# Performance work log

Hardware: AMD Instinct MI355X
Metric: run time of the kernel (lower is better)

The kernel has to match this reference:

```python
import jax, jax.numpy as jnp
import numpy as np

N, E, D, H = 100000, 1600000, 128, 2  # nodes, edges, channels (in=out), heads
NEG_SLOPE = 0.2
EPS = 1e-16


def setup_inputs() -> dict:
    key = jax.random.key(0)
    ks = jax.random.split(key, 12)
    s = 1.0 / np.sqrt(D)
    return {
        "x": jax.random.normal(ks[0], (N, D), jnp.float32),
        "edge_index": jax.random.randint(ks[1], (2, E), 0, N, jnp.int64),
        "gamma": jnp.ones((D,), jnp.float32),
        "beta": jnp.zeros((D,), jnp.float32),
        "Wl": jax.random.normal(ks[2], (D, H * D), jnp.float32) * s,
        "bl": jnp.zeros((H * D,), jnp.float32),
        "Wr": jax.random.normal(ks[3], (D, H * D), jnp.float32) * s,
        "br": jnp.zeros((H * D,), jnp.float32),
        "att": jax.random.normal(ks[4], (H, D), jnp.float32) * s,
        "res_W": jax.random.normal(ks[5], (D, D), jnp.float32) * s,
        "bias": jnp.zeros((D,), jnp.float32),
    }


def _segment_softmax(alpha, seg, num_segments):
    m = jax.ops.segment_max(alpha, seg, num_segments=num_segments)
    a = jnp.exp(alpha - m[seg])
    z = jax.ops.segment_sum(a, seg, num_segments=num_segments)
    return a / (z[seg] + EPS)


def reference(x, edge_index, gamma, beta, Wl, bl, Wr, br, att, res_W, bias):
    n = x.shape[0]
    residual = x
    # per-node LayerNorm -> ReLU
    mu = x.mean(-1, keepdims=True)
    var = ((x - mu) ** 2).mean(-1, keepdims=True)
    h = (x - mu) * jax.lax.rsqrt(var + 1e-5) * gamma + beta
    h = jax.nn.relu(h)
    # GATv2: per-node linear transforms [N,H,D]
    xl = (h @ Wl + bl).reshape(n, H, D)  # source-side
    xr = (h @ Wr + br).reshape(n, H, D)  # target-side
    src, dst = edge_index[0], edge_index[1]
    e = jax.nn.leaky_relu(xl[src] + xr[dst], NEG_SLOPE)  # [E,H,D]
    alpha = jnp.einsum('ehd,hd->eh', e, att)             # [E,H]
    alpha = _segment_softmax(alpha, dst, n)
    msg = xl[src] * alpha[..., None]                     # [E,H,D]
    out = jax.ops.segment_sum(msg, dst, num_segments=n)  # [N,H,D]
    out = out.mean(axis=1)                               # concat=False -> mean heads
    out = out + h @ res_W + bias                         # GATv2 internal residual + bias
    return residual + out
```

## Files before the change

kernel.cpp:

```cpp
#include <hip/hip_runtime.h>
#include <hip/hip_bf16.h>
#include <cstdint>
#include <cstddef>

#define DCH 128
#define NHEADS 2
#define NEG_SLOPE 0.2f

typedef __attribute__((ext_vector_type(8))) short short8v;
typedef __attribute__((ext_vector_type(4))) float f32x4;
typedef __attribute__((ext_vector_type(2))) float f32x2;
typedef __attribute__((ext_vector_type(4))) int int4v;
typedef _Float16 h4 __attribute__((ext_vector_type(4)));

__device__ __forceinline__ unsigned short f2bf(float f) {
    union { float f; unsigned int i; } v; v.f = f;
    unsigned int r = v.i + 0x7fffu + ((v.i >> 16) & 1u);
    return (unsigned short)(r >> 16);
}
__device__ __forceinline__ unsigned short f2h_bits(float f) {
    _Float16 h = (_Float16)f;
    union { _Float16 h; unsigned short u; } v; v.h = h; return v.u;
}

__device__ __forceinline__ float halfsum(float p) {
    p += __int_as_float(__builtin_amdgcn_update_dpp(
            0, __float_as_int(p), 0x121, 0xF, 0xF, false));
    p += __int_as_float(__builtin_amdgcn_update_dpp(
            0, __float_as_int(p), 0x122, 0xF, 0xF, false));
    p += __int_as_float(__builtin_amdgcn_update_dpp(
            0, __float_as_int(p), 0x124, 0xF, 0xF, false));
    p += __int_as_float(__builtin_amdgcn_update_dpp(
            0, __float_as_int(p), 0x128, 0xF, 0xF, false));
    p += __int_as_float(__builtin_amdgcn_ds_swizzle(
            __float_as_int(p), 0x401F));
    return p;
}

__global__ void prep_hist(const float* __restrict__ Wl, const float* __restrict__ Wr,
                          const float* __restrict__ resW,
                          unsigned short* __restrict__ wfrag,
                          const int* __restrict__ dst, int* __restrict__ cnt, int E) {
    if (blockIdx.x >= 40) {
        int i = (blockIdx.x - 40) * 256 + threadIdx.x;
        int E4 = E >> 2;
        if (i < E4) {
            int4 d = ((const int4*)dst)[i];
            atomicAdd(&cnt[d.x], 1); atomicAdd(&cnt[d.y], 1);
            atomicAdd(&cnt[d.z], 1); atomicAdd(&cnt[d.w], 1);
        }
        if (i < (E & 3)) atomicAdd(&cnt[dst[E4 * 4 + i]], 1);
        return;
    }
    int gid  = blockIdx.x * 256 + threadIdx.x;
    int lane = gid & 63;
    int f    = gid >> 6;
    int ks   = f & 3;
    int ct   = f >> 2;
    int col  = ct * 16 + (lane & 15);
    int k0   = ks * 32 + (lane >> 4) * 8;
    const float* W; int ldB, c;
    if (col < 256)      { W = Wl;   ldB = 256; c = col; }
    else if (col < 512) { W = Wr;   ldB = 256; c = col - 256; }
    else                { W = resW; ldB = 128; c = col - 512; }
    unsigned short tmp[8];
#pragma unroll
    for (int j = 0; j < 8; ++j) tmp[j] = f2bf(W[(size_t)(k0 + j) * ldB + c]);
    ushort4* dstp = (ushort4*)(wfrag + (size_t)gid * 8);
    dstp[0] = make_ushort4(tmp[0], tmp[1], tmp[2], tmp[3]);
    dstp[1] = make_ushort4(tmp[4], tmp[5], tmp[6], tmp[7]);
}

__launch_bounds__(256)
__global__ void gemm_fill(const float* __restrict__ x,
                          const float* __restrict__ gamma, const float* __restrict__ beta,
                          const unsigned short* __restrict__ wfrag,
                          const float* __restrict__ bl, const float* __restrict__ br,
                          const float* __restrict__ bias,
                          unsigned char* __restrict__ xl8, unsigned short* __restrict__ xr,
                          float* __restrict__ out, int n,
                          const int* __restrict__ srcIdx, const int* __restrict__ dstIdx,
                          int* __restrict__ fillc, int* __restrict__ sbuf, int E, int nrb) {
    __shared__ __align__(16) unsigned char smem[128 * 256];

    if ((int)blockIdx.x >= nrb) {
        int i = (blockIdx.x - nrb) * 256 + threadIdx.x;
        int E4 = E >> 2;
        if (i < E4) {
            int4 d = ((const int4*)dstIdx)[i];
            int4 s = ((const int4*)srcIdx)[i];
            sbuf[atomicAdd(&fillc[d.x], 1)] = s.x;
            sbuf[atomicAdd(&fillc[d.y], 1)] = s.y;
            sbuf[atomicAdd(&fillc[d.z], 1)] = s.z;
            sbuf[atomicAdd(&fillc[d.w], 1)] = s.w;
        }
        if (i < (E & 3)) {
            int e = E4 * 4 + i;
            sbuf[atomicAdd(&fillc[dstIdx[e]], 1)] = srcIdx[e];
        }
        return;
    }

    int row0 = blockIdx.x * 128;
    int tid  = threadIdx.x;
    unsigned short* As = (unsigned short*)smem;

    {
        int r  = tid >> 5;
        int k4 = (tid & 31) * 4;
        float4 g4  = *(const float4*)(gamma + k4);
        float4 be4 = *(const float4*)(beta + k4);
#pragma unroll
        for (int i = 0; i < 16; ++i) {
            int row  = r + i * 8;
            int grow = row0 + row;
            float4 a = (grow < n) ? *(const float4*)(x + (size_t)grow * DCH + k4)
                                  : make_float4(0.f, 0.f, 0.f, 0.f);
            float s  = a.x + a.y + a.z + a.w;
            float sq = a.x * a.x + a.y * a.y + a.z * a.z + a.w * a.w;
#pragma unroll
            for (int msk = 16; msk; msk >>= 1) {
                s  += __shfl_xor(s, msk);
                sq += __shfl_xor(sq, msk);
            }
            float mu = s * (1.f / DCH);
            float rs = rsqrtf(sq * (1.f / DCH) - mu * mu + 1e-5f);
            ushort4 u;
            u.x = f2bf(fmaxf((a.x - mu) * rs * g4.x + be4.x, 0.f));
            u.y = f2bf(fmaxf((a.y - mu) * rs * g4.y + be4.y, 0.f));
            u.z = f2bf(fmaxf((a.z - mu) * rs * g4.z + be4.z, 0.f));
            u.w = f2bf(fmaxf((a.w - mu) * rs * g4.w + be4.w, 0.f));
            int byteoff = row * 256 + ((k4 * 2) ^ ((row & 7) << 4));
            *(ushort4*)((char*)As + byteoff) = u;
        }
    }
    __syncthreads();

    int wv = tid >> 6, lane = tid & 63;

    short8v afrag[2][4];
#pragma unroll
    for (int g = 0; g < 2; ++g) {
        int arow = wv * 32 + g * 16 + (lane & 15);
#pragma unroll
        for (int ks = 0; ks < 4; ++ks) {
            int kbyte = (ks * 64 + (lane >> 4) * 16) ^ ((arow & 7) << 4);
            afrag[g][ks] = *(const short8v*)((const char*)As + arow * 256 + kbyte);
        }
    }
    __syncthreads();

    int nodeL0 = wv * 32 + (lane & 15);
    int nodeL1 = nodeL0 + 16;
    int cq = (lane >> 4) << 2;

    auto mfma_ct = [&](int ct, f32x4& a0, f32x4& a1) {
        const unsigned short* bp = wfrag + ((size_t)(ct * 4) * 64 + lane) * 8;
        short8v b0 = *(const short8v*)(bp);
        short8v b1 = *(const short8v*)(bp + 64 * 8);
        short8v b2 = *(const short8v*)(bp + 128 * 8);
        short8v b3 = *(const short8v*)(bp + 192 * 8);
        a0 = __builtin_amdgcn_mfma_f32_16x16x32_bf16(b0, afrag[0][0], a0, 0, 0, 0);
        a1 = __builtin_amdgcn_mfma_f32_16x16x32_bf16(b0, afrag[1][0], a1, 0, 0, 0);
        a0 = __builtin_amdgcn_mfma_f32_16x16x32_bf16(b1, afrag[0][1], a0, 0, 0, 0);
        a1 = __builtin_amdgcn_mfma_f32_16x16x32_bf16(b1, afrag[1][1], a1, 0, 0, 0);
        a0 = __builtin_amdgcn_mfma_f32_16x16x32_bf16(b2, afrag[0][2], a0, 0, 0, 0);
        a1 = __builtin_amdgcn_mfma_f32_16x16x32_bf16(b2, afrag[1][2], a1, 0, 0, 0);
        a0 = __builtin_amdgcn_mfma_f32_16x16x32_bf16(b3, afrag[0][3], a0, 0, 0, 0);
        a1 = __builtin_amdgcn_mfma_f32_16x16x32_bf16(b3, afrag[1][3], a1, 0, 0, 0);
    };

    {
#pragma unroll
        for (int ct = 0; ct < 16; ++ct) {
            f32x4 a0 = {0,0,0,0}, a1 = {0,0,0,0};
            mfma_ct(ct, a0, a1);
            int c = ct * 16 + cq;
            float4 bb = *(const float4*)(bl + c);
            int cb = ct * 16 + cq;
            int p0 = __builtin_amdgcn_cvt_pk_fp8_f32(a0[0] + bb.x, a0[1] + bb.y, 0, false);
            p0     = __builtin_amdgcn_cvt_pk_fp8_f32(a0[2] + bb.z, a0[3] + bb.w, p0, true);
            *(int*)(smem + nodeL0 * 256 + (cb ^ ((nodeL0 & 7) << 4))) = p0;
            int p1 = __builtin_amdgcn_cvt_pk_fp8_f32(a1[0] + bb.x, a1[1] + bb.y, 0, false);
            p1     = __builtin_amdgcn_cvt_pk_fp8_f32(a1[2] + bb.z, a1[3] + bb.w, p1, true);
            *(int*)(smem + nodeL1 * 256 + (cb ^ ((nodeL1 & 7) << 4))) = p1;
        }
        __syncthreads();
#pragma unroll
        for (int it = 0; it < 8; ++it) {
            int chunk = it * 256 + tid;
            int row  = chunk >> 4;
            int colb = (chunk & 15) * 16;
            int grow = row0 + row;
            if (grow < n) {
                int4v v = *(const int4v*)(smem + row * 256 + (colb ^ ((row & 7) << 4)));
                *(int4v*)(xl8 + (size_t)grow * 256 + colb) = v;
            }
        }
        __syncthreads();
    }

    for (int fg = 0; fg < 2; ++fg) {
#pragma unroll
        for (int ctl = 0; ctl < 8; ++ctl) {
            int ct = 16 + fg * 8 + ctl;
            f32x4 a0 = {0,0,0,0}, a1 = {0,0,0,0};
            mfma_ct(ct, a0, a1);
            int c = ct * 16 + cq - 256;
            float4 bb = *(const float4*)(br + c);
            int cb = ctl * 32 + cq * 2;
            ushort4 u0 = make_ushort4(f2h_bits(a0[0] + bb.x), f2h_bits(a0[1] + bb.y),
                                      f2h_bits(a0[2] + bb.z), f2h_bits(a0[3] + bb.w));
            *(ushort4*)(smem + nodeL0 * 256 + (cb ^ ((nodeL0 & 7) << 4))) = u0;
            ushort4 u1 = make_ushort4(f2h_bits(a1[0] + bb.x), f2h_bits(a1[1] + bb.y),
                                      f2h_bits(a1[2] + bb.z), f2h_bits(a1[3] + bb.w));
            *(ushort4*)(smem + nodeL1 * 256 + (cb ^ ((nodeL1 & 7) << 4))) = u1;
        }
        __syncthreads();
#pragma unroll
        for (int it = 0; it < 8; ++it) {
            int chunk = it * 256 + tid;
            int row  = chunk >> 4;
            int colb = (chunk & 15) * 16;
            int grow = row0 + row;
            if (grow < n) {
                int4v v = *(const int4v*)(smem + row * 256 + (colb ^ ((row & 7) << 4)));
                __builtin_nontemporal_store(v,
                    (int4v*)((char*)xr + (size_t)grow * 512 + fg * 256 + colb));
            }
        }
        __syncthreads();
    }

    for (int fg = 0; fg < 2; ++fg) {
#pragma unroll
        for (int ctl = 0; ctl < 4; ++ctl) {
            int ct = 32 + fg * 4 + ctl;
            f32x4 a0 = {0,0,0,0}, a1 = {0,0,0,0};
            mfma_ct(ct, a0, a1);
            int c = ct * 16 + cq - 512;
            float4 bb = *(const float4*)(bias + c);
            int cb = ctl * 64 + cq * 4;
            float4 w0 = make_float4(a0[0] + bb.x, a0[1] + bb.y,
                                    a0[2] + bb.z, a0[3] + bb.w);
            *(float4*)(smem + nodeL0 * 256 + (cb ^ ((nodeL0 & 7) << 4))) = w0;
            float4 w1 = make_float4(a1[0] + bb.x, a1[1] + bb.y,
                                    a1[2] + bb.z, a1[3] + bb.w);
            *(float4*)(smem + nodeL1 * 256 + (cb ^ ((nodeL1 & 7) << 4))) = w1;
        }
        __syncthreads();
#pragma unroll
        for (int it = 0; it < 8; ++it) {
            int chunk = it * 256 + tid;
            int row  = chunk >> 4;
            int colb = (chunk & 15) * 16;
            int grow = row0 + row;
            if (grow < n) {
                f32x4 v = *(const f32x4*)(smem + row * 256 + (colb ^ ((row & 7) << 4)));
                const float* xp = (const float*)((const char*)x + (size_t)grow * 512 + fg * 256 + colb);
                f32x4 xv = *(const f32x4*)xp;
                v = v + xv;
                __builtin_nontemporal_store(v,
                    (f32x4*)((char*)out + (size_t)grow * 512 + fg * 256 + colb));
            }
        }
        __syncthreads();
    }
}

__global__ void scan_block(const int* __restrict__ cnt, int* __restrict__ offs,
                           int* __restrict__ bsum, int n) {
    __shared__ int sm[256];
    int t = threadIdx.x;
    int i = blockIdx.x * 256 + t;
    int v = (i < n) ? cnt[i] : 0;
    sm[t] = v;
    __syncthreads();
#pragma unroll
    for (int d = 1; d < 256; d <<= 1) {
        int add = (t >= d) ? sm[t - d] : 0;
        __syncthreads();
        sm[t] += add;
        __syncthreads();
    }
    if (i < n) offs[i] = sm[t] - v;
    if (t == 255) bsum[blockIdx.x] = sm[t];
}

__global__ void scan_bsum_par(int* __restrict__ bsum, int nb) {
    __shared__ int sm[512];
    int t = threadIdx.x;
    if (nb <= 512) {
        int v = (t < nb) ? bsum[t] : 0;
        sm[t] = v;
        __syncthreads();
#pragma unroll
        for (int d = 1; d < 512; d <<= 1) {
            int add = (t >= d) ? sm[t - d] : 0;
            __syncthreads();
            sm[t] += add;
            __syncthreads();
        }
        if (t < nb) bsum[t] = sm[t] - v;
    } else if (t == 0) {
        int acc = 0;
        for (int i = 0; i < nb; ++i) { int v = bsum[i]; bsum[i] = acc; acc += v; }
    }
}

__global__ void scan_add(int* __restrict__ offs, int* __restrict__ fillc,
                         const int* __restrict__ bsum, int n, int E) {
    int i = blockIdx.x * 256 + threadIdx.x;
    if (i < n) {
        int v = offs[i] + bsum[blockIdx.x];
        offs[i]  = v;
        fillc[i] = v;
    }
    if (i == 0) offs[n] = E;
}

__launch_bounds__(256)
__global__ void gat_aggregate(const int* __restrict__ offs, const int* __restrict__ sbuf,
                              const unsigned char* __restrict__ xl8,
                              const unsigned short* __restrict__ xr_,
                              const float* __restrict__ att,
                              float* __restrict__ out, int n) {
    const _Float16* xr = (const _Float16*)xr_;
    int lane = threadIdx.x & 63;
    int wid  = __builtin_amdgcn_readfirstlane((blockIdx.x * blockDim.x + threadIdx.x) >> 6);
    int nw   = (gridDim.x * blockDim.x) >> 6;

    const float LOG2E = 1.4426950408889634f;
    float4 af = *(const float4*)(att + lane * 4);
    float ax = af.x * LOG2E, ay = af.y * LOG2E, az = af.z * LOG2E, aw = af.w * LOG2E;

    for (int t = wid; t < n; t += nw) {
        int beg = offs[t];
        int end = offs[t + 1];
        if (beg == end) continue;
        h4 rr = *(const h4*)(xr + (size_t)t * 256 + lane * 4);
        float rx = (float)rr[0], ry = (float)rr[1], rz = (float)rr[2], rw = (float)rr[3];

        float m = -INFINITY, z = 0.f;
        float4 acc = make_float4(0.f, 0.f, 0.f, 0.f);

        auto process4 = [&](int u0, int u1, int u2, int u3) {
            f32x2 l0a = __builtin_amdgcn_cvt_pk_f32_fp8(u0, false);
            f32x2 l0b = __builtin_amdgcn_cvt_pk_f32_fp8(u0, true);
            f32x2 l1a = __builtin_amdgcn_cvt_pk_f32_fp8(u1, false);
            f32x2 l1b = __builtin_amdgcn_cvt_pk_f32_fp8(u1, true);
            f32x2 l2a = __builtin_amdgcn_cvt_pk_f32_fp8(u2, false);
            f32x2 l2b = __builtin_amdgcn_cvt_pk_f32_fp8(u2, true);
            f32x2 l3a = __builtin_amdgcn_cvt_pk_f32_fp8(u3, false);
            f32x2 l3b = __builtin_amdgcn_cvt_pk_f32_fp8(u3, true);

            auto logit = [&](f32x2 la, f32x2 lb) {
                float vx = la.x + rx; vx = fmaxf(vx, NEG_SLOPE * vx);
                float vy = la.y + ry; vy = fmaxf(vy, NEG_SLOPE * vy);
                float vz = lb.x + rz; vz = fmaxf(vz, NEG_SLOPE * vz);
                float vw = lb.y + rw; vw = fmaxf(vw, NEG_SLOPE * vw);
                return fmaf(vw, aw, fmaf(vz, az, fmaf(vy, ay, vx * ax)));
            };
            float p0 = halfsum(logit(l0a, l0b));
            float p1 = halfsum(logit(l1a, l1b));
            float p2 = halfsum(logit(l2a, l2b));
            float p3 = halfsum(logit(l3a, l3b));
            float pm = fmaxf(fmaxf(p0, p1), fmaxf(p2, p3));
            if (__any(pm - m > 11.5f)) {
                float mn = fmaxf(m, pm);
                float sc = __builtin_amdgcn_exp2f(m - mn);
                z *= sc;
                acc.x *= sc; acc.y *= sc; acc.z *= sc; acc.w *= sc;
                m = mn;
            }
            float w0 = __builtin_amdgcn_exp2f(p0 - m);
            float w1 = __builtin_amdgcn_exp2f(p1 - m);
            float w2 = __builtin_amdgcn_exp2f(p2 - m);
            float w3 = __builtin_amdgcn_exp2f(p3 - m);
            z += (w0 + w1) + (w2 + w3);
            acc.x = fmaf(l0a.x, w0, acc.x); acc.y = fmaf(l0a.y, w0, acc.y);
            acc.z = fmaf(l0b.x, w0, acc.z); acc.w = fmaf(l0b.y, w0, acc.w);
            acc.x = fmaf(l1a.x, w1, acc.x); acc.y = fmaf(l1a.y, w1, acc.y);
            acc.z = fmaf(l1b.x, w1, acc.z); acc.w = fmaf(l1b.y, w1, acc.w);
            acc.x = fmaf(l2a.x, w2, acc.x); acc.y = fmaf(l2a.y, w2, acc.y);
            acc.z = fmaf(l2b.x, w2, acc.z); acc.w = fmaf(l2b.y, w2, acc.w);
            acc.x = fmaf(l3a.x, w3, acc.x); acc.y = fmaf(l3a.y, w3, acc.y);
            acc.z = fmaf(l3b.x, w3, acc.z); acc.w = fmaf(l3b.y, w3, acc.w);
        };

        int j = beg;
        int c0, c1, c2, c3;
        int d0, d1, d2, d3;
        bool haveC = (j + 4 <= end);
        if (haveC) {
            int s0 = sbuf[j], s1 = sbuf[j + 1], s2 = sbuf[j + 2], s3 = sbuf[j + 3];
            c0 = *(const int*)(xl8 + (size_t)s0 * 256 + lane * 4);
            c1 = *(const int*)(xl8 + (size_t)s1 * 256 + lane * 4);
            c2 = *(const int*)(xl8 + (size_t)s2 * 256 + lane * 4);
            c3 = *(const int*)(xl8 + (size_t)s3 * 256 + lane * 4);
        }
        bool haveD = (j + 8 <= end);
        if (haveD) {
            int s0 = sbuf[j + 4], s1 = sbuf[j + 5], s2 = sbuf[j + 6], s3 = sbuf[j + 7];
            d0 = *(const int*)(xl8 + (size_t)s0 * 256 + lane * 4);
            d1 = *(const int*)(xl8 + (size_t)s1 * 256 + lane * 4);
            d2 = *(const int*)(xl8 + (size_t)s2 * 256 + lane * 4);
            d3 = *(const int*)(xl8 + (size_t)s3 * 256 + lane * 4);
        }
        for (; j + 12 <= end; j += 4) {
            int s0 = sbuf[j + 8], s1 = sbuf[j + 9], s2 = sbuf[j + 10], s3 = sbuf[j + 11];
            int n0 = *(const int*)(xl8 + (size_t)s0 * 256 + lane * 4);
            int n1 = *(const int*)(xl8 + (size_t)s1 * 256 + lane * 4);
            int n2 = *(const int*)(xl8 + (size_t)s2 * 256 + lane * 4);
            int n3 = *(const int*)(xl8 + (size_t)s3 * 256 + lane * 4);
            process4(c0, c1, c2, c3);
            c0 = d0; c1 = d1; c2 = d2; c3 = d3;
            d0 = n0; d1 = n1; d2 = n2; d3 = n3;
        }
        if (haveD) {
            process4(c0, c1, c2, c3);
            c0 = d0; c1 = d1; c2 = d2; c3 = d3;
            j += 4;
        }
        if (haveC) {
            process4(c0, c1, c2, c3);
            j += 4;
        }
        for (; j < end; ++j) {
            int u = *(const int*)(xl8 + (size_t)sbuf[j] * 256 + lane * 4);
            f32x2 la = __builtin_amdgcn_cvt_pk_f32_fp8(u, false);
            f32x2 lb = __builtin_amdgcn_cvt_pk_f32_fp8(u, true);
            float vx = la.x + rx; vx = fmaxf(vx, NEG_SLOPE * vx);
            float vy = la.y + ry; vy = fmaxf(vy, NEG_SLOPE * vy);
            float vz = lb.x + rz; vz = fmaxf(vz, NEG_SLOPE * vz);
            float vw = lb.y + rw; vw = fmaxf(vw, NEG_SLOPE * vw);
            float p = halfsum(fmaf(vw, aw, fmaf(vz, az, fmaf(vy, ay, vx * ax))));
            if (__any(p - m > 11.5f)) {
                float mn = fmaxf(m, p);
                float sc = __builtin_amdgcn_exp2f(m - mn);
                z *= sc;
                acc.x *= sc; acc.y *= sc; acc.z *= sc; acc.w *= sc;
                m = mn;
            }
            float w = __builtin_amdgcn_exp2f(p - m);
            z += w;
            acc.x = fmaf(la.x, w, acc.x); acc.y = fmaf(la.y, w, acc.y);
            acc.z = fmaf(lb.x, w, acc.z); acc.w = fmaf(lb.y, w, acc.w);
        }
        float inv = 0.5f / (z + 1e-16f);
        acc.x *= inv; acc.y *= inv; acc.z *= inv; acc.w *= inv;
        acc.x += __shfl_xor(acc.x, 32);
        acc.y += __shfl_xor(acc.y, 32);
        acc.z += __shfl_xor(acc.z, 32);
        acc.w += __shfl_xor(acc.w, 32);
        if (lane < 32) {
            float4* o = (float4*)(out + (size_t)t * DCH + lane * 4);
            float4 cur = *o;
            cur.x += acc.x; cur.y += acc.y; cur.z += acc.z; cur.w += acc.w;
            *o = cur;
        }
    }
}

extern "C" void kernel_launch(void* const* d_in, const int* in_sizes, int n_in,
                              void* d_out, int out_size, void* d_ws, size_t ws_size,
                              hipStream_t stream) {
    const float* x     = (const float*)d_in[0];
    const int*   ei    = (const int*)d_in[1];
    const float* gamma = (const float*)d_in[2];
    const float* beta  = (const float*)d_in[3];
    const float* Wl    = (const float*)d_in[4];
    const float* bl    = (const float*)d_in[5];
    const float* Wr    = (const float*)d_in[6];
    const float* br    = (const float*)d_in[7];
    const float* att   = (const float*)d_in[8];
    const float* resW  = (const float*)d_in[9];
    const float* bias  = (const float*)d_in[10];
    float* out = (float*)d_out;

    int n = in_sizes[0] / DCH;
    int E = in_sizes[1] / 2;
    const int* src = ei;
    const int* dstIdx = ei + E;

    char* ws = (char*)d_ws;
    size_t off = 0;
    auto alloc = [&](size_t bytes) -> void* {
        void* p = ws + off;
        off = (off + bytes + 255) & ~(size_t)255;
        return p;
    };

    int nb = (n + 255) / 256;

    unsigned char*  xl8 = (unsigned char*)alloc((size_t)n * 256);
    unsigned short* xr  = (unsigned short*)alloc((size_t)n * 256 * 2);
    unsigned short* wfrag = (unsigned short*)alloc(160 * 64 * 8 * 2);
    int* cnt   = (int*)alloc((size_t)n * 4);
    int* offs  = (int*)alloc((size_t)(n + 1) * 4);
    int* bsum  = (int*)alloc((size_t)nb * 4);
    int* fillc = (int*)alloc((size_t)n * 4);
    int* sbuf  = (int*)alloc((size_t)E * 4);

    (void)hipMemsetAsync(cnt, 0, (size_t)n * 4, stream);
    int ethr = (E / 4 + 255) / 256 + 1;
    prep_hist<<<40 + ethr, 256, 0, stream>>>(Wl, Wr, resW, wfrag, dstIdx, cnt, E);
    scan_block<<<nb, 256, 0, stream>>>(cnt, offs, bsum, n);
    scan_bsum_par<<<1, 512, 0, stream>>>(bsum, nb);
    scan_add<<<nb, 256, 0, stream>>>(offs, fillc, bsum, n, E);

    int nrb = (n + 127) / 128;
    gemm_fill<<<nrb + ethr, 256, 0, stream>>>(x, gamma, beta, wfrag, bl, br, bias,
                                              xl8, xr, out, n,
                                              src, dstIdx, fillc, sbuf, E, nrb);
    gat_aggregate<<<2048, 256, 0, stream>>>(offs, sbuf, xl8, xr, att, out, n);
}
```

Measured before the change: 290.7 us.

## Overlap edge histogram with GEMM and run CSR fill standalone

Moves the per-destination degree histogram out of the weight-prep kernel and into the GEMM kernel's extra blocks. The CSR fill becomes its own kernel that runs after the scan. This swaps which edge pass overlaps with the dense GEMM: the cheaper histogram now hides behind GEMM, while the heavier scatter fill runs alone. Weight prep becomes a small separate launch, which adds one kernel launch.

New measurement: 355.9 us. +22.4%, slower.

```diff
diff --git a/kernel.cpp b/kernel.cpp
--- a/kernel.cpp
+++ b/kernel.cpp
@@ -37,21 +37,9 @@
     return p;
 }
 
-__global__ void prep_hist(const float* __restrict__ Wl, const float* __restrict__ Wr,
-                          const float* __restrict__ resW,
-                          unsigned short* __restrict__ wfrag,
-                          const int* __restrict__ dst, int* __restrict__ cnt, int E) {
-    if (blockIdx.x >= 40) {
-        int i = (blockIdx.x - 40) * 256 + threadIdx.x;
-        int E4 = E >> 2;
-        if (i < E4) {
-            int4 d = ((const int4*)dst)[i];
-            atomicAdd(&cnt[d.x], 1); atomicAdd(&cnt[d.y], 1);
-            atomicAdd(&cnt[d.z], 1); atomicAdd(&cnt[d.w], 1);
-        }
-        if (i < (E & 3)) atomicAdd(&cnt[dst[E4 * 4 + i]], 1);
-        return;
-    }
+__global__ void prep_wfrag(const float* __restrict__ Wl, const float* __restrict__ Wr,
+                           const float* __restrict__ resW,
+                           unsigned short* __restrict__ wfrag) {
     int gid  = blockIdx.x * 256 + threadIdx.x;
     int lane = gid & 63;
     int f    = gid >> 6;
@@ -72,15 +60,15 @@
 }
 
 __launch_bounds__(256)
-__global__ void gemm_fill(const float* __restrict__ x,
+__global__ void gemm_hist(const float* __restrict__ x,
                           const float* __restrict__ gamma, const float* __restrict__ beta,
                           const unsigned short* __restrict__ wfrag,
                           const float* __restrict__ bl, const float* __restrict__ br,
                           const float* __restrict__ bias,
                           unsigned char* __restrict__ xl8, unsigned short* __restrict__ xr,
                           float* __restrict__ out, int n,
-                          const int* __restrict__ srcIdx, const int* __restrict__ dstIdx,
-                          int* __restrict__ fillc, int* __restrict__ sbuf, int E, int nrb) {
+                          const int* __restrict__ dstIdx, int* __restrict__ cnt,
+                          int E, int nrb) {
     __shared__ __align__(16) unsigned char smem[128 * 256];
 
     if ((int)blockIdx.x >= nrb) {
@@ -88,16 +76,10 @@
         int E4 = E >> 2;
         if (i < E4) {
             int4 d = ((const int4*)dstIdx)[i];
-            int4 s = ((const int4*)srcIdx)[i];
-            sbuf[atomicAdd(&fillc[d.x], 1)] = s.x;
-            sbuf[atomicAdd(&fillc[d.y], 1)] = s.y;
-            sbuf[atomicAdd(&fillc[d.z], 1)] = s.z;
-            sbuf[atomicAdd(&fillc[d.w], 1)] = s.w;
-        }
-        if (i < (E & 3)) {
-            int e = E4 * 4 + i;
-            sbuf[atomicAdd(&fillc[dstIdx[e]], 1)] = srcIdx[e];
-        }
+            atomicAdd(&cnt[d.x], 1); atomicAdd(&cnt[d.y], 1);
+            atomicAdd(&cnt[d.z], 1); atomicAdd(&cnt[d.w], 1);
+        }
+        if (i < (E & 3)) atomicAdd(&cnt[dstIdx[E4 * 4 + i]], 1);
         return;
     }
 
@@ -317,6 +299,24 @@
         fillc[i] = v;
     }
     if (i == 0) offs[n] = E;
+}
+
+__global__ void fill_csr(const int* __restrict__ src, const int* __restrict__ dst,
+                         int* __restrict__ fillc, int* __restrict__ sbuf, int E) {
+    int i = blockIdx.x * blockDim.x + threadIdx.x;
+    int E4 = E >> 2;
+    if (i < E4) {
+        int4 d = ((const int4*)dst)[i];
+        int4 s = ((const int4*)src)[i];
+        sbuf[atomicAdd(&fillc[d.x], 1)] = s.x;
+        sbuf[atomicAdd(&fillc[d.y], 1)] = s.y;
+        sbuf[atomicAdd(&fillc[d.z], 1)] = s.z;
+        sbuf[atomicAdd(&fillc[d.w], 1)] = s.w;
+    }
+    if (i < (E & 3)) {
+        int e = E4 * 4 + i;
+        sbuf[atomicAdd(&fillc[dst[e]], 1)] = src[e];
+    }
 }
 
 __launch_bounds__(256)
@@ -503,15 +503,15 @@
     int* sbuf  = (int*)alloc((size_t)E * 4);
 
     (void)hipMemsetAsync(cnt, 0, (size_t)n * 4, stream);
+    prep_wfrag<<<40, 256, 0, stream>>>(Wl, Wr, resW, wfrag);
+
+    int nrb = (n + 127) / 128;
     int ethr = (E / 4 + 255) / 256 + 1;
-    prep_hist<<<40 + ethr, 256, 0, stream>>>(Wl, Wr, resW, wfrag, dstIdx, cnt, E);
+    gemm_hist<<<nrb + ethr, 256, 0, stream>>>(x, gamma, beta, wfrag, bl, br, bias,
+                                              xl8, xr, out, n, dstIdx, cnt, E, nrb);
     scan_block<<<nb, 256, 0, stream>>>(cnt, offs, bsum, n);
     scan_bsum_par<<<1, 512, 0, stream>>>(bsum, nb);
     scan_add<<<nb, 256, 0, stream>>>(offs, fillc, bsum, n, E);
-
-    int nrb = (n + 127) / 128;
-    gemm_fill<<<nrb + ethr, 256, 0, stream>>>(x, gamma, beta, wfrag, bl, br, bias,
-                                              xl8, xr, out, n,
-                                              src, dstIdx, fillc, sbuf, E, nrb);
+    fill_csr<<<ethr, 256, 0, stream>>>(src, dstIdx, fillc, sbuf, E);
     gat_aggregate<<<2048, 256, 0, stream>>>(offs, sbuf, xl8, xr, att, out, n);
 }
```

## Split CSR fill by destination half and overlap second half with aggregation

Applied to the files above, without the earlier changes.

The CSR fill is split in two by destination node. The first half is filled alongside the GEMM. The second half is filled by extra blocks in a new fused kernel that at the same time aggregates the first-half nodes, and a final kernel then aggregates the second half. The aim is to hide the atomic scatter cost behind aggregation work. In exchange, the edge lists are read twice and there is one more kernel launch.

After: 308.1 us. 6.0% more time.

```diff
diff --git a/kernel.cpp b/kernel.cpp
--- a/kernel.cpp
+++ b/kernel.cpp
@@ -80,7 +80,8 @@
                           unsigned char* __restrict__ xl8, unsigned short* __restrict__ xr,
                           float* __restrict__ out, int n,
                           const int* __restrict__ srcIdx, const int* __restrict__ dstIdx,
-                          int* __restrict__ fillc, int* __restrict__ sbuf, int E, int nrb) {
+                          int* __restrict__ fillc, int* __restrict__ sbuf, int E,
+                          int nrb, int nhalf) {
     __shared__ __align__(16) unsigned char smem[128 * 256];
 
     if ((int)blockIdx.x >= nrb) {
@@ -89,14 +90,15 @@
         if (i < E4) {
             int4 d = ((const int4*)dstIdx)[i];
             int4 s = ((const int4*)srcIdx)[i];
-            sbuf[atomicAdd(&fillc[d.x], 1)] = s.x;
-            sbuf[atomicAdd(&fillc[d.y], 1)] = s.y;
-            sbuf[atomicAdd(&fillc[d.z], 1)] = s.z;
-            sbuf[atomicAdd(&fillc[d.w], 1)] = s.w;
+            if (d.x < nhalf) sbuf[atomicAdd(&fillc[d.x], 1)] = s.x;
+            if (d.y < nhalf) sbuf[atomicAdd(&fillc[d.y], 1)] = s.y;
+            if (d.z < nhalf) sbuf[atomicAdd(&fillc[d.z], 1)] = s.z;
+            if (d.w < nhalf) sbuf[atomicAdd(&fillc[d.w], 1)] = s.w;
         }
         if (i < (E & 3)) {
             int e = E4 * 4 + i;
-            sbuf[atomicAdd(&fillc[dstIdx[e]], 1)] = srcIdx[e];
+            int d = dstIdx[e];
+            if (d < nhalf) sbuf[atomicAdd(&fillc[d], 1)] = srcIdx[e];
         }
         return;
     }
@@ -319,22 +321,16 @@
     if (i == 0) offs[n] = E;
 }
 
-__launch_bounds__(256)
-__global__ void gat_aggregate(const int* __restrict__ offs, const int* __restrict__ sbuf,
-                              const unsigned char* __restrict__ xl8,
-                              const unsigned short* __restrict__ xr_,
-                              const float* __restrict__ att,
-                              float* __restrict__ out, int n) {
-    const _Float16* xr = (const _Float16*)xr_;
-    int lane = threadIdx.x & 63;
-    int wid  = __builtin_amdgcn_readfirstlane((blockIdx.x * blockDim.x + threadIdx.x) >> 6);
-    int nw   = (gridDim.x * blockDim.x) >> 6;
-
+__device__ __forceinline__ void gat_range(
+        const int* __restrict__ offs, const int* __restrict__ sbuf,
+        const unsigned char* __restrict__ xl8, const _Float16* __restrict__ xr,
+        const float* __restrict__ att, float* __restrict__ out,
+        int t0, int t1, int wid, int nw, int lane) {
     const float LOG2E = 1.4426950408889634f;
     float4 af = *(const float4*)(att + lane * 4);
     float ax = af.x * LOG2E, ay = af.y * LOG2E, az = af.z * LOG2E, aw = af.w * LOG2E;
 
-    for (int t = wid; t < n; t += nw) {
+    for (int t = t0 + wid; t < t1; t += nw) {
         int beg = offs[t];
         int end = offs[t + 1];
         if (beg == end) continue;
@@ -462,6 +458,50 @@
     }
 }
 
+__launch_bounds__(256)
+__global__ void gat_fill(const int* __restrict__ offs, const int* __restrict__ sbuf,
+                         const unsigned char* __restrict__ xl8,
+                         const unsigned short* __restrict__ xr_,
+                         const float* __restrict__ att, float* __restrict__ out,
+                         const int* __restrict__ srcIdx, const int* __restrict__ dstIdx,
+                         int* __restrict__ fillc, int* __restrict__ sbufW,
+                         int E, int nhalf, int GB) {
+    if ((int)blockIdx.x >= GB) {
+        int i = (blockIdx.x - GB) * 256 + threadIdx.x;
+        int E4 = E >> 2;
+        if (i < E4) {
+            int4 d = ((const int4*)dstIdx)[i];
+            int4 s = ((const int4*)srcIdx)[i];
+            if (d.x >= nhalf) sbufW[atomicAdd(&fillc[d.x], 1)] = s.x;
+            if (d.y >= nhalf) sbufW[atomicAdd(&fillc[d.y], 1)] = s.y;
+            if (d.z >= nhalf) sbufW[atomicAdd(&fillc[d.z], 1)] = s.z;
+            if (d.w >= nhalf) sbufW[atomicAdd(&fillc[d.w], 1)] = s.w;
+        }
+        if (i < (E & 3)) {
+            int e = E4 * 4 + i;
+            int d = dstIdx[e];
+            if (d >= nhalf) sbufW[atomicAdd(&fillc[d], 1)] = srcIdx[e];
+        }
+        return;
+    }
+    int lane = threadIdx.x & 63;
+    int wid  = __builtin_amdgcn_readfirstlane((blockIdx.x * 256 + threadIdx.x) >> 6);
+    int nw   = GB * 4;
+    gat_range(offs, sbuf, xl8, (const _Float16*)xr_, att, out, 0, nhalf, wid, nw, lane);
+}
+
+__launch_bounds__(256)
+__global__ void gat_aggregate(const int* __restrict__ offs, const int* __restrict__ sbuf,
+                              const unsigned char* __restrict__ xl8,
+                              const unsigned short* __restrict__ xr_,
+                              const float* __restrict__ att,
+                              float* __restrict__ out, int t0, int t1) {
+    int lane = threadIdx.x & 63;
+    int wid  = __builtin_amdgcn_readfirstlane((blockIdx.x * blockDim.x + threadIdx.x) >> 6);
+    int nw   = (gridDim.x * blockDim.x) >> 6;
+    gat_range(offs, sbuf, xl8, (const _Float16*)xr_, att, out, t0, t1, wid, nw, lane);
+}
+
 extern "C" void kernel_launch(void* const* d_in, const int* in_sizes, int n_in,
                               void* d_out, int out_size, void* d_ws, size_t ws_size,
                               hipStream_t stream) {
@@ -509,9 +549,13 @@
     scan_bsum_par<<<1, 512, 0, stream>>>(bsum, nb);
     scan_add<<<nb, 256, 0, stream>>>(offs, fillc, bsum, n, E);
 
+    int nhalf = n / 2;
     int nrb = (n + 127) / 128;
     gemm_fill<<<nrb + ethr, 256, 0, stream>>>(x, gamma, beta, wfrag, bl, br, bias,
                                               xl8, xr, out, n,
-                                              src, dstIdx, fillc, sbuf, E, nrb);
-    gat_aggregate<<<2048, 256, 0, stream>>>(offs, sbuf, xl8, xr, att, out, n);
-}
+                                              src, dstIdx, fillc, sbuf, E, nrb, nhalf);
+    int GB = 1024;
+    gat_fill<<<GB + ethr, 256, 0, stream>>>(offs, sbuf, xl8, xr, att, out,
+                                            src, dstIdx, fillc, sbuf, E, nhalf, GB);
+    gat_aggregate<<<2048, 256, 0, stream>>>(offs, sbuf, xl8, xr, att, out, nhalf, n);
+}
```
